# Performance work log

Hardware: AMD Instinct MI355X
Metric: run time of the kernel (lower is better)

The kernel has to match this reference:

```python
import jax, jax.numpy as jnp
import numpy as np

B, T, NODES, DEG = 16, 50, 62, 8
IN, C, H, NC, K = 64, 128, 256, 3, 5
G = B * T            # num_graphs
N = G * NODES        # total nodes
E = G * NODES * DEG  # total edges (before self loops)


def setup_inputs() -> dict:
    key = jax.random.key(0)
    ks = jax.random.split(key, 12)
    # random within-graph edges, PyG-batched with node offsets
    rng = np.random.RandomState(0)
    src = rng.randint(0, NODES, size=(G, NODES * DEG))
    dst = rng.randint(0, NODES, size=(G, NODES * DEG))
    off = (np.arange(G) * NODES)[:, None]
    edge_index = jnp.asarray(np.stack([(src + off).ravel(), (dst + off).ravel()]), dtype=jnp.int32)

    def glorot(k, shape, fan_in):
        return jax.random.normal(k, shape, jnp.float32) / np.sqrt(fan_in)

    return {
        "x": jax.random.normal(ks[0], (N, IN), jnp.float32),
        "edge_index": edge_index,
        "edge_attr": jax.random.normal(ks[1], (E, 1), jnp.float32),
        "W_l": glorot(ks[2], (IN, C), IN), "b_l": jnp.zeros((C,), jnp.float32),
        "W_r": glorot(ks[3], (IN, C), IN), "b_r": jnp.zeros((C,), jnp.float32),
        "W_e": glorot(ks[4], (1, C), 1),
        "att": glorot(ks[5], (C,), C),
        "bias_out": jnp.zeros((C,), jnp.float32),
        "W_ih": glorot(ks[6], (3 * H, C), C), "W_hh": glorot(ks[7], (3 * H, H), H),
        "b_ih": jnp.zeros((3 * H,), jnp.float32), "b_hh": jnp.zeros((3 * H,), jnp.float32),
        "W1": glorot(ks[8], (H, H // 2), H), "b1": jnp.zeros((H // 2,), jnp.float32),
        "W2": glorot(ks[9], (H // 2, NC), H // 2), "b2": jnp.zeros((NC,), jnp.float32),
    }


def _forward(x, edge_index, edge_attr, W_l, b_l, W_r, b_r, W_e, att, bias_out,
             W_ih, W_hh, b_ih, b_hh, W1, b1, W2, b2):
    n = x.shape[0]
    src, dst = edge_index[0], edge_index[1]

    # --- GATv2Conv: add self loops with edge_attr fill_value='mean' (PyG default) ---
    sum_attr = jax.ops.segment_sum(edge_attr, dst, num_segments=n)
    cnt = jax.ops.segment_sum(jnp.ones_like(dst, jnp.float32), dst, num_segments=n)
    loop_attr = sum_attr / jnp.clip(cnt, 1.0)[:, None]
    ar = jnp.arange(n, dtype=src.dtype)
    src2 = jnp.concatenate([src, ar])
    dst2 = jnp.concatenate([dst, ar])
    ea = jnp.concatenate([edge_attr, loop_attr], axis=0)

    xl = x @ W_l + b_l          # source-side transform
    xr = x @ W_r + b_r          # target-side transform
    ee = ea @ W_e               # edge embedding (lin_edge, bias=False)

    m = xl[src2] + xr[dst2] + ee                # [E2, C]
    e = jax.nn.leaky_relu(m, 0.2) @ att         # [E2]
    # scatter-softmax over incoming edges per target node (self loops => no empty segs)
    emax = jax.ops.segment_max(e, dst2, num_segments=n)
    ez = jnp.exp(e - emax[dst2])
    den = jax.ops.segment_sum(ez, dst2, num_segments=n)
    alpha = ez / den[dst2]                      # [E2]
    h_sp = jax.ops.segment_sum(alpha[:, None] * xl[src2], dst2, num_segments=n) + bias_out

    # --- mean pool per graph (uniform graph size => reshape) ---
    g = h_sp.reshape(G, NODES, C).mean(axis=1).reshape(B, T, C)

    # --- GRU (PyTorch gate order r, z, n) ---
    def step(h, xt):
        gx = xt @ W_ih.T + b_ih
        gh = h @ W_hh.T + b_hh
        xr_, xz, xn = jnp.split(gx, 3, axis=-1)
        hr, hz, hn = jnp.split(gh, 3, axis=-1)
        r = jax.nn.sigmoid(xr_ + hr)
        z = jax.nn.sigmoid(xz + hz)
        nn_ = jnp.tanh(xn + r * hn)
        h2 = (1.0 - z) * nn_ + z * h
        return h2, h2

    h0 = jnp.zeros((B, H), g.dtype)
    _, hs = jax.lax.scan(step, h0, jnp.swapaxes(g, 0, 1))  # [T,B,H]
    gru_out = jnp.swapaxes(hs, 0, 1)                       # [B,T,H]

    # --- classifier (dropout inactive at eval) ---
    scores = jax.nn.relu(gru_out @ W1 + b1) @ W2 + b2      # [B,T,NC]

    # --- top-k over time per class, then mean over k ---
    vals, idx = jax.lax.top_k(jnp.swapaxes(scores, 1, 2), K)  # [B,NC,K]
    return vals.mean(axis=-1), jnp.swapaxes(idx, 1, 2)        # [B,NC], [B,K,NC]


def reference(x, edge_index, edge_attr, W_l, b_l, W_r, b_r, W_e, att, bias_out,
              W_ih, W_hh, b_ih, b_hh, W1, b1, W2, b2):
    return _forward(x, edge_index, edge_attr, W_l, b_l, W_r, b_r, W_e, att, bias_out,
                    W_ih, W_hh, b_ih, b_hh, W1, b1, W2, b2)
```

## Files before the change

kernel.cpp:

```cpp
#include <hip/hip_runtime.h>
#include <math.h>

#define NNODES 62
#define NDEG 8
#define NGRAPH 800
#define NB 16
#define NT 50
#define NIN 64
#define NCH 128
#define NH 256
#define NCLS 3
#define NTOPK 5
#define NSL 16
#define EPG (NNODES*NDEG)
#define E2G (EPG + NNODES)
#define NTOTAL (NGRAPH*NNODES)
#define ETOTAL (NGRAPH*EPG)
#define NXB (NTOTAL/64)
#define TTB 96

__device__ __forceinline__ void load_lds_1k(const void* g, void* lds, int lane) {
    __builtin_amdgcn_global_load_lds(
        (const __attribute__((address_space(1))) unsigned int*)((const char*)g + lane * 16),
        (__attribute__((address_space(3))) unsigned int*)lds, 16, 0, 0);
}

__launch_bounds__(512, 4)
__global__ void k_xrl(const float* __restrict__ x,
                      const float* __restrict__ W_r, const float* __restrict__ b_r,
                      const float* __restrict__ W_l, const float* __restrict__ b_l,
                      const float* __restrict__ W_ih, float* __restrict__ W_ihT,
                      float* __restrict__ xr, float* __restrict__ xl) {
    __shared__ __align__(16) float x_s[64 * NIN];
    __shared__ __align__(16) float wr_s[NIN * NCH];
    __shared__ __align__(16) float wl_s[NIN * NCH];
    const int blk = blockIdx.x;
    const int tid = threadIdx.x;
    if (blk >= NXB) {
        for (int idx = (blk - NXB) * 512 + tid; idx < 3 * NH * NCH; idx += TTB * 512) {
            int r = idx / NCH, c = idx - r * NCH;
            W_ihT[c * (3 * NH) + r] = W_ih[idx];
        }
        return;
    }
    const int base_v = blk * 64;

    {
        const int wid = tid >> 6, lane = tid & 63;
        const char* xg = (const char*)(x + (size_t)base_v * NIN);
        #pragma unroll
        for (int c0 = 0; c0 < 10; ++c0) {
            int c = wid * 10 + c0;
            if (c < 32)
                load_lds_1k((const char*)W_r + c * 1024, (char*)wr_s + c * 1024, lane);
            else if (c < 64)
                load_lds_1k((const char*)W_l + (c - 32) * 1024, (char*)wl_s + (c - 32) * 1024, lane);
            else
                load_lds_1k(xg + (c - 64) * 1024, (char*)x_s + (c - 64) * 1024, lane);
        }
    }
    __syncthreads();

    const int c4 = (tid & 31) * 4;
    const int ng = tid >> 5;
    float4 aR[4], aL[4];
    float4 br4 = *reinterpret_cast<const float4*>(b_r + c4);
    float4 bl4 = *reinterpret_cast<const float4*>(b_l + c4);
    #pragma unroll
    for (int j = 0; j < 4; ++j) { aR[j] = br4; aL[j] = bl4; }

    const float* xs = x_s + (ng * 4) * NIN;
    for (int k4 = 0; k4 < NIN; k4 += 4) {
        float4 xv[4];
        #pragma unroll
        for (int j = 0; j < 4; ++j)
            xv[j] = *reinterpret_cast<const float4*>(&xs[j * NIN + k4]);
        #pragma unroll
        for (int kk = 0; kk < 4; ++kk) {
            float4 wr = *reinterpret_cast<const float4*>(&wr_s[(k4 + kk) * NCH + c4]);
            float4 wl = *reinterpret_cast<const float4*>(&wl_s[(k4 + kk) * NCH + c4]);
            #pragma unroll
            for (int j = 0; j < 4; ++j) {
                float xk = (kk == 0) ? xv[j].x : (kk == 1) ? xv[j].y
                         : (kk == 2) ? xv[j].z : xv[j].w;
                aR[j].x += xk * wr.x; aR[j].y += xk * wr.y;
                aR[j].z += xk * wr.z; aR[j].w += xk * wr.w;
                aL[j].x += xk * wl.x; aL[j].y += xk * wl.y;
                aL[j].z += xk * wl.z; aL[j].w += xk * wl.w;
            }
        }
    }
    #pragma unroll
    for (int j = 0; j < 4; ++j) {
        int v = base_v + ng * 4 + j;
        *reinterpret_cast<float4*>(xr + (size_t)v * NCH + c4) = aR[j];
        *reinterpret_cast<float4*>(xl + (size_t)v * NCH + c4) = aL[j];
    }
}

__launch_bounds__(256, 4)
__global__ void k_gat(const int* __restrict__ ei, const float* __restrict__ eattr,
                      const float* __restrict__ W_e, const float* __restrict__ att,
                      const float* __restrict__ bias_out,
                      const float* __restrict__ xr_all, const float* __restrict__ xl_all,
                      float* __restrict__ g_all) {
    __shared__ __align__(16) float xl_s[NNODES * NCH];
    __shared__ unsigned short csr_src[E2G];
    __shared__ float csr_attr[E2G];
    __shared__ float csr_e[E2G];
    __shared__ unsigned short off_s[NNODES + 2];
    __shared__ unsigned cur_s[NNODES];
    __shared__ unsigned cnt_s[NNODES];
    __shared__ float asum_s[NNODES];
    __shared__ float la_s[NNODES];
    __shared__ float gacc_s[4 * NCH];

    const int g = blockIdx.x;
    const int tid = threadIdx.x;
    const int base_e = g * EPG;
    const int base_n = g * NNODES;

    {
        const int wid = tid >> 6, lane = tid & 63;
        const char* src = (const char*)(xl_all + (size_t)base_n * NCH);
        for (int c = wid; c < 31; c += 4)
            load_lds_1k(src + c * 1024, (char*)xl_s + c * 1024, lane);
    }
    for (int v = tid; v < NNODES; v += 256) { asum_s[v] = 0.f; cnt_s[v] = 0u; cur_s[v] = 0u; }
    int s0 = -1, d0 = 0, s1 = -1, d1 = 0;
    float a0 = 0.f, a1 = 0.f;
    {
        int j0 = tid * 2, j1 = tid * 2 + 1;
        if (j0 < EPG) { s0 = ei[base_e + j0] - base_n; d0 = ei[ETOTAL + base_e + j0] - base_n; a0 = eattr[base_e + j0]; }
        if (j1 < EPG) { s1 = ei[base_e + j1] - base_n; d1 = ei[ETOTAL + base_e + j1] - base_n; a1 = eattr[base_e + j1]; }
    }
    __syncthreads();

    if (s0 >= 0) { atomicAdd(&cnt_s[d0], 1u); atomicAdd(&asum_s[d0], a0); }
    if (s1 >= 0) { atomicAdd(&cnt_s[d1], 1u); atomicAdd(&asum_s[d1], a1); }
    __syncthreads();

    if (tid < 64) {
        unsigned val = (tid < NNODES) ? (cnt_s[tid] + 1u) : 0u;
        unsigned xsc = val;
        #pragma unroll
        for (int dlt = 1; dlt < 64; dlt <<= 1) {
            unsigned o = __shfl_up(xsc, dlt, 64);
            if (tid >= dlt) xsc += o;
        }
        if (tid < NNODES) {
            off_s[tid] = (unsigned short)(xsc - val);
            la_s[tid] = asum_s[tid] / fmaxf((float)cnt_s[tid], 1.f);
        }
        if (tid == NNODES - 1) off_s[NNODES] = (unsigned short)xsc;
    }
    __syncthreads();

    if (s0 >= 0) { int sl = off_s[d0] + (int)atomicAdd(&cur_s[d0], 1u); csr_src[sl] = (unsigned short)s0; csr_attr[sl] = a0; }
    if (s1 >= 0) { int sl = off_s[d1] + (int)atomicAdd(&cur_s[d1], 1u); csr_src[sl] = (unsigned short)s1; csr_attr[sl] = a1; }
    if (tid < NNODES) { int sl = off_s[tid + 1] - 1; csr_src[sl] = (unsigned short)tid; csr_attr[sl] = la_s[tid]; }
    __syncthreads();

    const int wave = tid >> 6;
    const int lane = tid & 63;
    const int sub = lane & 15;
    const int gslot = wave * 4 + (lane >> 4);
    const int cb = sub * 8;

    float we0[8], at0[8];
    #pragma unroll
    for (int i = 0; i < 8; ++i) { we0[i] = W_e[cb + i]; at0[i] = att[cb + i]; }

    float acc[8];
    #pragma unroll
    for (int i = 0; i < 8; ++i) acc[i] = 0.f;

    for (int v = gslot; v < NNODES; v += 16) {
        const float* xrp = xr_all + (size_t)(base_n + v) * NCH + cb;
        float4 xr0 = *reinterpret_cast<const float4*>(xrp);
        float4 xr1 = *reinterpret_cast<const float4*>(xrp + 4);
        const int lo = off_s[v], hi = off_s[v + 1];
        float m = -INFINITY, ssum = 0.f;
        for (int sl = lo; sl < hi; ++sl) {
            int src = csr_src[sl];
            float a = csr_attr[sl];
            float4 x0 = *reinterpret_cast<const float4*>(&xl_s[src * NCH + cb]);
            float4 x1 = *reinterpret_cast<const float4*>(&xl_s[src * NCH + cb + 4]);
            float mi, t = 0.f;
            mi = x0.x + xr0.x + a * we0[0]; t += (mi >= 0.f ? mi : 0.2f * mi) * at0[0];
            mi = x0.y + xr0.y + a * we0[1]; t += (mi >= 0.f ? mi : 0.2f * mi) * at0[1];
            mi = x0.z + xr0.z + a * we0[2]; t += (mi >= 0.f ? mi : 0.2f * mi) * at0[2];
            mi = x0.w + xr0.w + a * we0[3]; t += (mi >= 0.f ? mi : 0.2f * mi) * at0[3];
            mi = x1.x + xr1.x + a * we0[4]; t += (mi >= 0.f ? mi : 0.2f * mi) * at0[4];
            mi = x1.y + xr1.y + a * we0[5]; t += (mi >= 0.f ? mi : 0.2f * mi) * at0[5];
            mi = x1.z + xr1.z + a * we0[6]; t += (mi >= 0.f ? mi : 0.2f * mi) * at0[6];
            mi = x1.w + xr1.w + a * we0[7]; t += (mi >= 0.f ? mi : 0.2f * mi) * at0[7];
            t += __shfl_xor(t, 1, 64);
            t += __shfl_xor(t, 2, 64);
            t += __shfl_xor(t, 4, 64);
            t += __shfl_xor(t, 8, 64);
            if (sub == 0) csr_e[sl] = t;
            float mn = fmaxf(m, t);
            ssum = ssum * __expf(m - mn) + __expf(t - mn);
            m = mn;
        }
        float inv = 1.f / ssum;
        for (int sl = lo; sl < hi; ++sl) {
            int src = csr_src[sl];
            float al = __expf(csr_e[sl] - m) * inv;
            float4 x0 = *reinterpret_cast<const float4*>(&xl_s[src * NCH + cb]);
            float4 x1 = *reinterpret_cast<const float4*>(&xl_s[src * NCH + cb + 4]);
            acc[0] += al * x0.x; acc[1] += al * x0.y;
            acc[2] += al * x0.z; acc[3] += al * x0.w;
            acc[4] += al * x1.x; acc[5] += al * x1.y;
            acc[6] += al * x1.z; acc[7] += al * x1.w;
        }
    }
    #pragma unroll
    for (int i = 0; i < 8; ++i) {
        acc[i] += __shfl_xor(acc[i], 16, 64);
        acc[i] += __shfl_xor(acc[i], 32, 64);
    }
    if ((lane >> 4) == 0) {
        *reinterpret_cast<float4*>(&gacc_s[wave * NCH + cb]) =
            make_float4(acc[0], acc[1], acc[2], acc[3]);
        *reinterpret_cast<float4*>(&gacc_s[wave * NCH + cb + 4]) =
            make_float4(acc[4], acc[5], acc[6], acc[7]);
    }
    __syncthreads();

    for (int c = tid; c < NCH; c += 256) {
        float v = (gacc_s[c] + gacc_s[NCH + c] + gacc_s[2 * NCH + c] + gacc_s[3 * NCH + c])
                      * (1.f / NNODES) + bias_out[c];
        g_all[(size_t)g * NCH + c] = v;
    }
}

__global__ void k_gx(const float* __restrict__ g_all, const float* __restrict__ W_ihT,
                     const float* __restrict__ b_ih, const float* __restrict__ b_hh,
                     float* __restrict__ gx_all, unsigned long long* __restrict__ h_pub) {
    if (blockIdx.x < 32)
        h_pub[(size_t)blockIdx.x * 256 + threadIdx.x] = 0ull;
    int idx = blockIdx.x * blockDim.x + threadIdx.x;
    if (idx >= NGRAPH * 3 * NH) return;
    int gi = idx / (3 * NH);
    int o = idx - gi * (3 * NH);
    float acc = b_ih[o] + (o < 2 * NH ? b_hh[o] : 0.f);
    const float* grow = g_all + (size_t)gi * NCH;
    for (int c = 0; c < NCH; ++c) acc += grow[c] * W_ihT[c * (3 * NH) + o];
    gx_all[idx] = acc;
}

__launch_bounds__(256, 1)
__global__ void k_gru(const float* __restrict__ gx_all, const float* __restrict__ W_hh,
                      const float* __restrict__ b_hh, float* __restrict__ h_all,
                      unsigned long long* __restrict__ h_pub) {
    __shared__ __align__(16) float h_s[NH];
    __shared__ float gh_s[48];
    __shared__ float gx_s[2][48];

    const int bid = blockIdx.x;
    const int b = bid >> 4;
    const int s = bid & 15;
    const int tid = threadIdx.x;
    const int wv = tid >> 6;
    const int g = tid >> 2;
    const int l = tid & 3;

    float4 Wv[16];
    if (tid < 192) {
        int row = (g < 16) ? (NSL * s + g)
                : (g < 32) ? (NH + NSL * s + (g - 16))
                           : (2 * NH + NSL * s + (g - 32));
        const float* wr = W_hh + (size_t)row * NH + 64 * l;
        #pragma unroll
        for (int j = 0; j < 16; ++j) {
            int jeff = (j + 2 * l) & 15;
            Wv[j] = *reinterpret_cast<const float4*>(wr + 4 * jeff);
        }
    }
    const float bhn = (tid < NSL) ? b_hh[2 * NH + NSL * s + tid] : 0.f;
    const int own_lo = NSL * s, own_hi = NSL * s + NSL;

    for (int i = tid; i < NH; i += 256) h_s[i] = 0.f;
    if (wv == 3) {
        int i = tid - 192;
        if (i < 48) {
            int o = (i < 16) ? (NSL * s + i) : (i < 32) ? (NH + NSL * s + i - 16)
                                                        : (2 * NH + NSL * s + i - 32);
            gx_s[0][i] = gx_all[(size_t)(b * NT + 0) * (3 * NH) + o];
        }
    }
    __syncthreads();

    for (int t = 0; t < NT; ++t) {
        if (wv == 3) {
            int i = tid - 192;
            if (i < 48 && t + 1 < NT) {
                int o = (i < 16) ? (NSL * s + i) : (i < 32) ? (NH + NSL * s + i - 16)
                                                            : (2 * NH + NSL * s + i - 32);
                gx_s[(t + 1) & 1][i] = gx_all[(size_t)(b * NT + t + 1) * (3 * NH) + o];
            }
        } else {
            float a0 = 0.f, a1 = 0.f, a2 = 0.f, a3 = 0.f;
            #pragma unroll
            for (int j = 0; j < 16; ++j) {
                int jeff = (j + 2 * l) & 15;
                float4 hv = *reinterpret_cast<const float4*>(&h_s[64 * l + 4 * jeff]);
                float4 w = Wv[j];
                a0 += w.x * hv.x; a1 += w.y * hv.y; a2 += w.z * hv.z; a3 += w.w * hv.w;
            }
            float acc = (a0 + a1) + (a2 + a3);
            acc += __shfl_xor(acc, 1, 64);
            acc += __shfl_xor(acc, 2, 64);
            if (l == 0) gh_s[g] = acc;
        }
        __syncthreads();

        const int par = (t + 1) & 1;
        if (tid < NSL) {
            const float* gx = gx_s[t & 1];
            float r = 1.f / (1.f + expf(-(gx[tid] + gh_s[tid])));
            float z = 1.f / (1.f + expf(-(gx[16 + tid] + gh_s[16 + tid])));
            float n = tanhf(gx[32 + tid] + r * (gh_s[32 + tid] + bhn));
            int o = own_lo + tid;
            float hv = (1.f - z) * n + z * h_s[o];
            h_all[(size_t)(b * NT + t) * NH + o] = hv;
            unsigned long long w = ((unsigned long long)(unsigned)(t + 1) << 32)
                                 | (unsigned long long)__float_as_uint(hv);
            __hip_atomic_store(&h_pub[((size_t)b * 2 + par) * NH + o], w,
                               __ATOMIC_RELAXED, __HIP_MEMORY_SCOPE_AGENT);
            h_s[o] = hv;
        }
        if (tid < own_lo || tid >= own_hi) {
            const unsigned long long* p = &h_pub[((size_t)b * 2 + par) * NH + tid];
            unsigned long long w;
            const unsigned target = (unsigned)(t + 1);
            while ((unsigned)((w = __hip_atomic_load(p, __ATOMIC_RELAXED,
                                                     __HIP_MEMORY_SCOPE_AGENT)) >> 32) != target)
                __builtin_amdgcn_s_sleep(1);
            h_s[tid] = __uint_as_float((unsigned)w);
        }
        __syncthreads();
    }
}

__launch_bounds__(128)
__global__ void k_cls(const float* __restrict__ h_all,
                      const float* __restrict__ W1, const float* __restrict__ b1,
                      const float* __restrict__ W2, const float* __restrict__ b2,
                      float* __restrict__ sc_all) {
    __shared__ float h_s[NH];
    __shared__ float s1_s[NH / 2];
    const int bt = blockIdx.x;
    const int tid = threadIdx.x;
    h_s[tid] = h_all[(size_t)bt * NH + tid];
    h_s[tid + 128] = h_all[(size_t)bt * NH + tid + 128];
    __syncthreads();
    float acc = b1[tid];
    #pragma unroll 8
    for (int k = 0; k < NH; ++k) acc += h_s[k] * W1[k * (NH / 2) + tid];
    s1_s[tid] = fmaxf(acc, 0.f);
    __syncthreads();
    if (tid < NCLS) {
        float a = b2[tid];
        for (int k = 0; k < NH / 2; ++k) a += s1_s[k] * W2[k * NCLS + tid];
        sc_all[bt * NCLS + tid] = a;
    }
}

__global__ void k_topk(const float* __restrict__ sc_all, float* __restrict__ out) {
    int tid = threadIdx.x;
    if (tid >= NB * NCLS) return;
    int b = tid / NCLS;
    int c = tid - b * NCLS;
    float vals[NT];
    for (int t = 0; t < NT; ++t) vals[t] = sc_all[(b * NT + t) * NCLS + c];
    float sum = 0.f;
    for (int k = 0; k < NTOPK; ++k) {
        float best = -INFINITY; int bi = 0;
        for (int t = 0; t < NT; ++t) {
            if (vals[t] > best) { best = vals[t]; bi = t; }
        }
        vals[bi] = -INFINITY;
        sum += best;
        out[NB * NCLS + b * (NTOPK * NCLS) + k * NCLS + c] = (float)bi;
    }
    out[b * NCLS + c] = sum * (1.f / NTOPK);
}

extern "C" void kernel_launch(void* const* d_in, const int* in_sizes, int n_in,
                              void* d_out, int out_size, void* d_ws, size_t ws_size,
                              hipStream_t stream) {
    const float* x        = (const float*)d_in[0];
    const int*   ei       = (const int*)  d_in[1];
    const float* eattr    = (const float*)d_in[2];
    const float* W_l      = (const float*)d_in[3];
    const float* b_l      = (const float*)d_in[4];
    const float* W_r      = (const float*)d_in[5];
    const float* b_r      = (const float*)d_in[6];
    const float* W_e      = (const float*)d_in[7];
    const float* att      = (const float*)d_in[8];
    const float* bias_out = (const float*)d_in[9];
    const float* W_ih     = (const float*)d_in[10];
    const float* W_hh     = (const float*)d_in[11];
    const float* b_ih     = (const float*)d_in[12];
    const float* b_hh     = (const float*)d_in[13];
    const float* W1       = (const float*)d_in[14];
    const float* b1       = (const float*)d_in[15];
    const float* W2       = (const float*)d_in[16];
    const float* b2       = (const float*)d_in[17];
    float* out = (float*)d_out;

    float* ws = (float*)d_ws;
    float* xr_all = ws;
    float* xl_all = xr_all + (size_t)NTOTAL * NCH;
    float* g_all  = xl_all + (size_t)NTOTAL * NCH;
    float* gx_all = g_all + NGRAPH * NCH;
    float* W_ihT  = gx_all + NGRAPH * 3 * NH;
    float* h_all  = W_ihT + NCH * 3 * NH;
    float* sc_all = h_all + (size_t)NGRAPH * NH;
    unsigned long long* h_pub = (unsigned long long*)xr_all;

    k_xrl<<<NXB + TTB, 512, 0, stream>>>(x, W_r, b_r, W_l, b_l, W_ih, W_ihT, xr_all, xl_all);
    k_gat<<<NGRAPH, 256, 0, stream>>>(ei, eattr, W_e, att, bias_out, xr_all, xl_all, g_all);
    k_gx<<<(NGRAPH * 3 * NH + 255) / 256, 256, 0, stream>>>(g_all, W_ihT, b_ih, b_hh,
                                                            gx_all, h_pub);
    k_gru<<<NB * NSL, 256, 0, stream>>>(gx_all, W_hh, b_hh, h_all, h_pub);
    k_cls<<<NB * NT, 128, 0, stream>>>(h_all, W1, b1, W2, b2, sc_all);
    k_topk<<<1, 64, 0, stream>>>(sc_all, out);
}
```

Measured before the change: 212.1 us.

## Publish raw gate pre-activations and compute GRU update redundantly in every block

The GRU step now publishes each block's partial W_hh·h dot products (r, z, n gates) to global memory instead of the final hidden slice. Every block then polls all 768 gate values and computes the full 256-wide hidden update itself. This removes the serial phase where 16 threads did the gate math before publishing, so the cross-block critical path per step becomes one publish and one poll. In exchange each thread polls three words instead of one, the publish buffer is three times larger, gx loads move into per-thread registers, and an extra barrier is added per step.

Result: slower. 261.0 us (+23.1%).

```diff
diff --git a/kernel.cpp b/kernel.cpp
--- a/kernel.cpp
+++ b/kernel.cpp
@@ -239,7 +239,7 @@
 __global__ void k_gx(const float* __restrict__ g_all, const float* __restrict__ W_ihT,
                      const float* __restrict__ b_ih, const float* __restrict__ b_hh,
                      float* __restrict__ gx_all, unsigned long long* __restrict__ h_pub) {
-    if (blockIdx.x < 32)
+    if (blockIdx.x < 96)
         h_pub[(size_t)blockIdx.x * 256 + threadIdx.x] = 0ull;
     int idx = blockIdx.x * blockDim.x + threadIdx.x;
     if (idx >= NGRAPH * 3 * NH) return;
@@ -256,14 +256,11 @@
                       const float* __restrict__ b_hh, float* __restrict__ h_all,
                       unsigned long long* __restrict__ h_pub) {
     __shared__ __align__(16) float h_s[NH];
-    __shared__ float gh_s[48];
-    __shared__ float gx_s[2][48];
 
     const int bid = blockIdx.x;
     const int b = bid >> 4;
     const int s = bid & 15;
     const int tid = threadIdx.x;
-    const int wv = tid >> 6;
     const int g = tid >> 2;
     const int l = tid & 3;
 
@@ -278,30 +275,29 @@
             int jeff = (j + 2 * l) & 15;
             Wv[j] = *reinterpret_cast<const float4*>(wr + 4 * jeff);
         }
-    }
-    const float bhn = (tid < NSL) ? b_hh[2 * NH + NSL * s + tid] : 0.f;
-    const int own_lo = NSL * s, own_hi = NSL * s + NSL;
-
-    for (int i = tid; i < NH; i += 256) h_s[i] = 0.f;
-    if (wv == 3) {
-        int i = tid - 192;
-        if (i < 48) {
-            int o = (i < 16) ? (NSL * s + i) : (i < 32) ? (NH + NSL * s + i - 16)
-                                                        : (2 * NH + NSL * s + i - 32);
-            gx_s[0][i] = gx_all[(size_t)(b * NT + 0) * (3 * NH) + o];
-        }
-    }
+        #pragma unroll
+        for (int j = 0; j < 16; ++j)
+            asm volatile("" : "+v"(Wv[j].x), "+v"(Wv[j].y), "+v"(Wv[j].z), "+v"(Wv[j].w));
+    }
+    const int pub_o = NSL * s + (g & 15);
+    const int pub_q = g >> 4;
+    const float bhn = b_hh[2 * NH + tid];
+
+    float gxr[2], gxz[2], gxn[2];
+    {
+        const float* gx = gx_all + (size_t)(b * NT) * (3 * NH);
+        gxr[0] = gx[tid]; gxz[0] = gx[tid + NH]; gxn[0] = gx[tid + 2 * NH];
+    }
+    h_s[tid] = 0.f;
     __syncthreads();
 
     for (int t = 0; t < NT; ++t) {
-        if (wv == 3) {
-            int i = tid - 192;
-            if (i < 48 && t + 1 < NT) {
-                int o = (i < 16) ? (NSL * s + i) : (i < 32) ? (NH + NSL * s + i - 16)
-                                                            : (2 * NH + NSL * s + i - 32);
-                gx_s[(t + 1) & 1][i] = gx_all[(size_t)(b * NT + t + 1) * (3 * NH) + o];
-            }
-        } else {
+        const int cur = t & 1, par = (t + 1) & 1;
+        if (t + 1 < NT) {
+            const float* gx = gx_all + (size_t)(b * NT + t + 1) * (3 * NH);
+            gxr[par] = gx[tid]; gxz[par] = gx[tid + NH]; gxn[par] = gx[tid + 2 * NH];
+        }
+        if (tid < 192) {
             float a0 = 0.f, a1 = 0.f, a2 = 0.f, a3 = 0.f;
             #pragma unroll
             for (int j = 0; j < 16; ++j) {
@@ -313,33 +309,37 @@
             float acc = (a0 + a1) + (a2 + a3);
             acc += __shfl_xor(acc, 1, 64);
             acc += __shfl_xor(acc, 2, 64);
-            if (l == 0) gh_s[g] = acc;
+            if (l == 0) {
+                unsigned long long w = ((unsigned long long)(unsigned)(t + 1) << 32)
+                                     | (unsigned long long)__float_as_uint(acc);
+                __hip_atomic_store(&h_pub[(((size_t)b * 2 + par) * NH + pub_o) * 3 + pub_q], w,
+                                   __ATOMIC_RELAXED, __HIP_MEMORY_SCOPE_AGENT);
+            }
         }
         __syncthreads();
 
-        const int par = (t + 1) & 1;
-        if (tid < NSL) {
-            const float* gx = gx_s[t & 1];
-            float r = 1.f / (1.f + expf(-(gx[tid] + gh_s[tid])));
-            float z = 1.f / (1.f + expf(-(gx[16 + tid] + gh_s[16 + tid])));
-            float n = tanhf(gx[32 + tid] + r * (gh_s[32 + tid] + bhn));
-            int o = own_lo + tid;
-            float hv = (1.f - z) * n + z * h_s[o];
-            h_all[(size_t)(b * NT + t) * NH + o] = hv;
-            unsigned long long w = ((unsigned long long)(unsigned)(t + 1) << 32)
-                                 | (unsigned long long)__float_as_uint(hv);
-            __hip_atomic_store(&h_pub[((size_t)b * 2 + par) * NH + o], w,
-                               __ATOMIC_RELAXED, __HIP_MEMORY_SCOPE_AGENT);
-            h_s[o] = hv;
-        }
-        if (tid < own_lo || tid >= own_hi) {
-            const unsigned long long* p = &h_pub[((size_t)b * 2 + par) * NH + tid];
-            unsigned long long w;
+        {
+            const unsigned long long* p = &h_pub[(((size_t)b * 2 + par) * NH + tid) * 3];
             const unsigned target = (unsigned)(t + 1);
-            while ((unsigned)((w = __hip_atomic_load(p, __ATOMIC_RELAXED,
-                                                     __HIP_MEMORY_SCOPE_AGENT)) >> 32) != target)
+            unsigned long long w0, w1, w2;
+            for (;;) {
+                w0 = __hip_atomic_load(p + 0, __ATOMIC_RELAXED, __HIP_MEMORY_SCOPE_AGENT);
+                w1 = __hip_atomic_load(p + 1, __ATOMIC_RELAXED, __HIP_MEMORY_SCOPE_AGENT);
+                w2 = __hip_atomic_load(p + 2, __ATOMIC_RELAXED, __HIP_MEMORY_SCOPE_AGENT);
+                if ((unsigned)(w0 >> 32) == target && (unsigned)(w1 >> 32) == target &&
+                    (unsigned)(w2 >> 32) == target) break;
                 __builtin_amdgcn_s_sleep(1);
-            h_s[tid] = __uint_as_float((unsigned)w);
+            }
+            float ghr = __uint_as_float((unsigned)w0);
+            float ghz = __uint_as_float((unsigned)w1);
+            float ghn = __uint_as_float((unsigned)w2);
+            float r = 1.f / (1.f + expf(-(gxr[cur] + ghr)));
+            float z = 1.f / (1.f + expf(-(gxz[cur] + ghz)));
+            float n = tanhf(gxn[cur] + r * (ghn + bhn));
+            float hv = (1.f - z) * n + z * h_s[tid];
+            if (s == 0) h_all[(size_t)(b * NT + t) * NH + tid] = hv;
+            __syncthreads();
+            h_s[tid] = hv;
         }
         __syncthreads();
     }
```
